# Performance work log

Measured on AMD Instinct MI355X. Metric: run time of the kernel, lower is better.

## Reference

```python
import math
import jax, jax.numpy as jnp
import numpy as np

B, L, D, H, DFF, T, V = 512, 128, 128, 4, 256, 2048, 20000
LN_EPS = 1e-5
LOG_SIGMA0 = math.log(0.1)


def _keygen(base):
    c = [0]
    def nk():
        k = jax.random.fold_in(base, c[0]); c[0] += 1
        return k
    return nk


def bayes_linear(x, wmu, wls, bmu, bls, nk):
    # weight = mu + exp(log_sigma) * eps (fresh eps every call, as in BayesLinear.forward)
    w = wmu + jnp.exp(wls) * jax.random.normal(nk(), wmu.shape, wmu.dtype)
    b = bmu + jnp.exp(bls) * jax.random.normal(nk(), bmu.shape, bmu.dtype)
    return jnp.einsum('...d,od->...o', x, w) + b


def layer_norm(x, g, b):
    m = x.mean(-1, keepdims=True)
    v = ((x - m) ** 2).mean(-1, keepdims=True)
    return (x - m) / jnp.sqrt(v + LN_EPS) * g + b


def mha(q, k, v, wmu, wls, bmu, bls, nk):
    # wmu: [4, D, D] for q, k, v, o projections
    dk = D // H
    def proj(x, i):
        return bayes_linear(x, wmu[i], wls[i], bmu[i], bls[i], nk)
    def split(x):
        return x.reshape(B, L, H, dk).transpose(0, 2, 1, 3)
    Q, K, Vh = split(proj(q, 0)), split(proj(k, 1)), split(proj(v, 2))
    probs = jax.nn.softmax(jnp.einsum('bhqd,bhkd->bhqk', Q, K) / math.sqrt(dk), axis=-1)
    out = jnp.einsum('bhqk,bhkd->bhqd', probs, Vh).transpose(0, 2, 1, 3).reshape(B, L, D)
    return bayes_linear(out, wmu[3], wls[3], bmu[3], bls[3], nk)


def setup_inputs() -> dict:
    key = jax.random.key(0)
    ks = iter(jax.random.split(key, 64))
    def u(shape, fan_in):
        s = 1.0 / math.sqrt(fan_in)
        return jax.random.uniform(next(ks), shape, jnp.float32, -s, s)
    def ls(shape):
        return jnp.full(shape, LOG_SIGMA0, jnp.float32)
    return dict(
        event_set=jax.random.randint(next(ks), (B, L), 0, V),
        time=jax.random.uniform(next(ks), (B, L), jnp.float32),
        mask=jax.random.randint(next(ks), (B, L), 0, L),
        set_size=jax.random.randint(next(ks), (B,), 1, L),
        emb=jax.random.normal(next(ks), (V, D), jnp.float32),
        dec_wmu=u((2, 8, D, D), D), dec_wls=ls((2, 8, D, D)),
        dec_bmu=u((2, 8, D), D), dec_bls=ls((2, 8, D)),
        ffn1_wmu=u((2, DFF, D), D), ffn1_wls=ls((2, DFF, D)),
        ffn1_bmu=u((2, DFF), D), ffn1_bls=ls((2, DFF)),
        ffn2_wmu=u((2, D, DFF), DFF), ffn2_wls=ls((2, D, DFF)),
        ffn2_bmu=u((2, D), DFF), ffn2_bls=ls((2, D)),
        ln_g=jnp.ones((2, 3, D), jnp.float32), ln_b=jnp.zeros((2, 3, D), jnp.float32),
        alpha_wmu=u((5, T, D), D), alpha_wls=ls((5, T, D)),
        alpha_bmu=u((5, T), D), alpha_bls=ls((5, T)),
        at_wmu=u((5, 1, D), D), at_wls=ls((5, 1, D)),
        at_bmu=u((5, 1), D), at_bls=ls((5, 1)),
        em_w=u((5, T, D), D), em_b=u((5, T), D),
        es_w=u((5, T, D), D), es_b=u((5, T), D),
        tm_w=u((5, 1, D), D), tm_b=u((5, 1), D),
        ts_w=u((5, 1, D), D), ts_b=u((5, 1), D),
    )


def reference(event_set, time, mask, set_size, emb,
              dec_wmu, dec_wls, dec_bmu, dec_bls,
              ffn1_wmu, ffn1_wls, ffn1_bmu, ffn1_bls,
              ffn2_wmu, ffn2_wls, ffn2_bmu, ffn2_bls,
              ln_g, ln_b, alpha_wmu, alpha_wls, alpha_bmu, alpha_bls,
              at_wmu, at_wls, at_bmu, at_bls,
              em_w, em_b, es_w, es_b, tm_w, tm_b, ts_w, ts_b):
    nk = _keygen(jax.random.key(42))
    x = emb[event_set]                                     # [B, L, D]
    # sinusoidal positional encoding driven by `mask` (integer positions)
    pos = mask.astype(jnp.float32)
    div = jnp.exp(jnp.arange(D, dtype=jnp.float32) * (-math.log(10000.0) / D))
    ang = pos[..., None] * div                             # [B, L, D]
    pos_enc = jnp.where((mask % 2 == 0)[..., None], jnp.sin(ang), jnp.cos(ang))
    inp_x = x + pos_enc
    # two decoder layers: self-attn on x, cross-attn against inp_x (dropout = eval identity)
    for l in range(2):
        a = mha(x, x, x, dec_wmu[l, :4], dec_wls[l, :4], dec_bmu[l, :4], dec_bls[l, :4], nk)
        x = layer_norm(x + a, ln_g[l, 0], ln_b[l, 0])
        a = mha(x, inp_x, inp_x, dec_wmu[l, 4:], dec_wls[l, 4:], dec_bmu[l, 4:], dec_bls[l, 4:], nk)
        x = layer_norm(x + a, ln_g[l, 1], ln_b[l, 1])
        h1 = jax.nn.relu(bayes_linear(x, ffn1_wmu[l], ffn1_wls[l], ffn1_bmu[l], ffn1_bls[l], nk))
        f = bayes_linear(h1, ffn2_wmu[l], ffn2_wls[l], ffn2_bmu[l], ffn2_bls[l], nk)
        x = layer_norm(x + f, ln_g[l, 2], ln_b[l, 2])
    h = x[:, 0, :]                                          # [B, D]
    # 5 Bayesian alpha heads -> softmax over mixture dim (vectorized over k)
    aw = alpha_wmu + jnp.exp(alpha_wls) * jax.random.normal(nk(), alpha_wmu.shape)
    ab = alpha_bmu + jnp.exp(alpha_bls) * jax.random.normal(nk(), alpha_bmu.shape)
    alpha = jax.nn.softmax(jnp.einsum('bd,ktd->btk', h, aw) + ab.T[None], axis=2)   # [B, T, 5]
    atw = at_wmu + jnp.exp(at_wls) * jax.random.normal(nk(), at_wmu.shape)
    atb = at_bmu + jnp.exp(at_bls) * jax.random.normal(nk(), at_bmu.shape)
    alpha_t = jax.nn.softmax(jnp.einsum('bd,kd->bk', h, atw[:, 0]) + atb[:, 0][None], axis=1)  # [B, 5]
    # mixture of 5 reparameterized Gaussian predictors (plain Linears)
    means = jnp.einsum('bd,ktd->bkt', h, em_w) + em_b[None]          # [B, 5, T]
    stds = jnp.exp(jnp.einsum('bd,ktd->bkt', h, es_w) + es_b[None])
    noise_e = jax.random.normal(nk(), (B, 5, T))
    event_pred = jnp.sum(jnp.swapaxes(alpha, 1, 2) * (means + stds * noise_e), axis=1)   # [B, T]
    tmeans = jnp.einsum('bd,kd->bk', h, tm_w[:, 0]) + tm_b[:, 0][None]                   # [B, 5]
    tstds = jnp.exp(jnp.einsum('bd,kd->bk', h, ts_w[:, 0]) + ts_b[:, 0][None])
    noise_t = jax.random.normal(nk(), (B, 5))
    time_pred = jnp.sum(alpha_t * (tmeans + tstds * noise_t), axis=1, keepdims=True)     # [B, 1]
    return event_pred, time_pred
```

## Files before the change

### kernel.cpp

```cpp
#include <hip/hip_runtime.h>
#include <cstdint>
#include <cstddef>


#define NB   512
#define NL   128
#define ND   128
#define NH   4
#define NDFF 256
#define NT   2048
#define BL   (NB * NL)

typedef __attribute__((ext_vector_type(8))) short bf16x8;
typedef __attribute__((ext_vector_type(4))) float f32x4;

#define MFMA16(a, b, c) __builtin_amdgcn_mfma_f32_16x16x32_bf16((a), (b), (c), 0, 0, 0)

__host__ __device__ __forceinline__ void tf2x32(uint32_t k0, uint32_t k1,
                                                uint32_t x0, uint32_t x1,
                                                uint32_t& o0, uint32_t& o1)
{
  const uint32_t ks2 = k0 ^ k1 ^ 0x1BD11BDAu;
  x0 += k0; x1 += k1;
#define TF_RND(r) { x0 += x1; x1 = (x1 << (r)) | (x1 >> (32 - (r))); x1 ^= x0; }
  TF_RND(13) TF_RND(15) TF_RND(26) TF_RND(6)
  x0 += k1;  x1 += ks2 + 1u;
  TF_RND(17) TF_RND(29) TF_RND(16) TF_RND(24)
  x0 += ks2; x1 += k0 + 2u;
  TF_RND(13) TF_RND(15) TF_RND(26) TF_RND(6)
  x0 += k0;  x1 += k1 + 3u;
  TF_RND(17) TF_RND(29) TF_RND(16) TF_RND(24)
  x0 += k1;  x1 += ks2 + 4u;
  TF_RND(13) TF_RND(15) TF_RND(26) TF_RND(6)
  x0 += ks2; x1 += k0 + 5u;
#undef TF_RND
  o0 = x0; o1 = x1;
}

__device__ __forceinline__ float erfinv32(float x)
{
  float w = -log1pf(-__fmul_rn(x, x));
  float p;
  if (w < 5.0f) {
    w = w - 2.5f;
    p = 2.81022636e-08f;
    p = __fadd_rn( 3.43273939e-07f, __fmul_rn(p, w));
    p = __fadd_rn(-3.5233877e-06f,  __fmul_rn(p, w));
    p = __fadd_rn(-4.39150654e-06f, __fmul_rn(p, w));
    p = __fadd_rn( 0.00021858087f,  __fmul_rn(p, w));
    p = __fadd_rn(-0.00125372503f,  __fmul_rn(p, w));
    p = __fadd_rn(-0.00417768164f,  __fmul_rn(p, w));
    p = __fadd_rn( 0.246640727f,    __fmul_rn(p, w));
    p = __fadd_rn( 1.50140941f,     __fmul_rn(p, w));
  } else {
    w = sqrtf(w) - 3.0f;
    p = -0.000200214257f;
    p = __fadd_rn( 0.000100950558f, __fmul_rn(p, w));
    p = __fadd_rn( 0.00134934322f,  __fmul_rn(p, w));
    p = __fadd_rn(-0.00367342844f,  __fmul_rn(p, w));
    p = __fadd_rn( 0.00573950773f,  __fmul_rn(p, w));
    p = __fadd_rn(-0.0076224613f,   __fmul_rn(p, w));
    p = __fadd_rn( 0.00943887047f,  __fmul_rn(p, w));
    p = __fadd_rn( 1.00167406f,     __fmul_rn(p, w));
    p = __fadd_rn( 2.83297682f,     __fmul_rn(p, w));
  }
  return __fmul_rn(p, x);
}

__device__ __forceinline__ float bits_to_normal(uint32_t bits)
{
  const float lo = -0.99999994f;
  float f = __uint_as_float((bits >> 9) | 0x3F800000u) - 1.0f;
  float u = __fadd_rn(__fmul_rn(f, 2.0f), lo);
  u = fmaxf(lo, u);
  return __fmul_rn(1.41421356f, erfinv32(u));
}

__device__ __forceinline__ float jax_normal_idx(uint32_t k0, uint32_t k1, uint32_t idx)
{
  uint32_t o0, o1;
  tf2x32(k0, k1, 0u, idx, o0, o1);
  return bits_to_normal(o0 ^ o1);
}

__device__ __forceinline__ ushort f2bf(float f)
{
  uint32_t u = __float_as_uint(f);
  u += 0x7fffu + ((u >> 16) & 1u);
  return (ushort)(u >> 16);
}

#define SA_DECB 262144
#define SA_F1W  264192
#define SA_F1B  329728
#define SA_F2W  330240
#define SA_F2B  395776
#define SA_AW   396032
#define SA_AB   1706752
#define SA_ATW  1716992
#define SA_ATB  1717632
#define SA_TOT  1717637

#define BW_DEC  0
#define BW_F1   262144
#define BW_F2   327680
#define BW_AW   393216
#define BW_TOT  1703936

#define BF_DECB 0
#define BF_F1B  2048
#define BF_F2B  2560
#define BF_AB   2816
#define BF_ATW  13056
#define BF_ATB  13696
#define BF_TOT  13701

__global__ __launch_bounds__(256) void sample_all_kernel(
    const float* __restrict__ dec_wmu, const float* __restrict__ dec_wls,
    const float* __restrict__ dec_bmu, const float* __restrict__ dec_bls,
    const float* __restrict__ f1_wmu,  const float* __restrict__ f1_wls,
    const float* __restrict__ f1_bmu,  const float* __restrict__ f1_bls,
    const float* __restrict__ f2_wmu,  const float* __restrict__ f2_wls,
    const float* __restrict__ f2_bmu,  const float* __restrict__ f2_bls,
    const float* __restrict__ a_wmu,   const float* __restrict__ a_wls,
    const float* __restrict__ a_bmu,   const float* __restrict__ a_bls,
    const float* __restrict__ at_wmu,  const float* __restrict__ at_wls,
    const float* __restrict__ at_bmu,  const float* __restrict__ at_bls,
    ushort* __restrict__ wbf, float* __restrict__ wf32)
{
  const int i = blockIdx.x * 256 + threadIdx.x;
  if (i >= SA_TOT) return;
  const float* mu; const float* ls;
  uint32_t c, idx;
  int bf_dst = -1, f32_dst = -1;
  if (i < SA_DECB) {
    int s = i >> 14;
    mu = dec_wmu + i; ls = dec_wls + i;
    c = 2u * s + (s >= 8 ? 4u : 0u); idx = (uint32_t)(i & 16383);
    bf_dst = BW_DEC + i;
  } else if (i < SA_F1W) {
    int t = i - SA_DECB; int s = t >> 7;
    mu = dec_bmu + t; ls = dec_bls + t;
    c = 2u * s + 1u + (s >= 8 ? 4u : 0u); idx = (uint32_t)(t & 127);
    f32_dst = BF_DECB + t;
  } else if (i < SA_F1B) {
    int t = i - SA_F1W; int s = t >> 15;
    mu = f1_wmu + t; ls = f1_wls + t;
    c = 16u + 20u * s; idx = (uint32_t)(t & 32767);
    bf_dst = BW_F1 + t;
  } else if (i < SA_F2W) {
    int t = i - SA_F1B; int s = t >> 8;
    mu = f1_bmu + t; ls = f1_bls + t;
    c = 17u + 20u * s; idx = (uint32_t)(t & 255);
    f32_dst = BF_F1B + t;
  } else if (i < SA_F2B) {
    int t = i - SA_F2W; int s = t >> 15;
    mu = f2_wmu + t; ls = f2_wls + t;
    c = 18u + 20u * s; idx = (uint32_t)(t & 32767);
    bf_dst = BW_F2 + t;
  } else if (i < SA_AW) {
    int t = i - SA_F2B; int s = t >> 7;
    mu = f2_bmu + t; ls = f2_bls + t;
    c = 19u + 20u * s; idx = (uint32_t)(t & 127);
    f32_dst = BF_F2B + t;
  } else if (i < SA_AB) {
    int t = i - SA_AW;
    mu = a_wmu + t; ls = a_wls + t; c = 40u; idx = (uint32_t)t;
    bf_dst = BW_AW + t;
  } else if (i < SA_ATW) {
    int t = i - SA_AB;
    mu = a_bmu + t; ls = a_bls + t; c = 41u; idx = (uint32_t)t;
    f32_dst = BF_AB + t;
  } else if (i < SA_ATB) {
    int t = i - SA_ATW;
    mu = at_wmu + t; ls = at_wls + t; c = 42u; idx = (uint32_t)t;
    f32_dst = BF_ATW + t;
  } else {
    int t = i - SA_ATB;
    mu = at_bmu + t; ls = at_bls + t; c = 43u; idx = (uint32_t)t;
    f32_dst = BF_ATB + t;
  }
  uint32_t k0, k1;
  tf2x32(0u, 42u, 0u, c, k0, k1);
  float v = mu[0] + expf(ls[0]) * jax_normal_idx(k0, k1, idx);
  if (bf_dst >= 0) wbf[bf_dst] = f2bf(v);
  else             wf32[f32_dst] = v;
}

#define STR 136

__global__ __launch_bounds__(512, 2) void decoder_mega_kernel(
    const int* __restrict__ ev, const int* __restrict__ mask,
    const float* __restrict__ emb,
    const ushort* __restrict__ WBF, const float* __restrict__ WF32,
    const float* __restrict__ lng_all, const float* __restrict__ lnb_all,
    float* __restrict__ Xh, ushort* __restrict__ Hb)
{
  __shared__ ushort WL[128][STR];
  __shared__ ushort Kt[128][STR];
  __shared__ ushort Vt[128][STR];
  __shared__ ushort Xb[128][STR];
  __shared__ ushort Ps[128][72];

  const int b = blockIdx.x;
  const int tid = threadIdx.x;
  const int w = tid >> 6, l = tid & 63;
  const int g = l >> 4, r16 = l & 15;
  const f32x4 zero = {0.f, 0.f, 0.f, 0.f};

  auto stageS = [&](ushort (*dst)[STR], const ushort* src, int srcStride) {
#pragma unroll
    for (int it = 0; it < 4; ++it) {
      int ci = tid + it * 512;
      int row = ci >> 4, q = ci & 15;
      *(bf16x8*)&dst[row][q * 8] = *(const bf16x8*)(src + (size_t)row * srcStride + q * 8);
    }
  };

  float xreg[8][4];
  {
    int ecr[4];
#pragma unroll
    for (int r = 0; r < 4; ++r) ecr[r] = ev[b * NL + 16 * w + 4 * g + r];
#pragma unroll
    for (int c = 0; c < 8; ++c)
#pragma unroll
      for (int r = 0; r < 4; ++r) {
        float x = emb[(size_t)ecr[r] * ND + 16 * c + r16];
        xreg[c][r] = x;
        Xb[16 * w + 4 * g + r][16 * c + r16] = f2bf(x);
      }
  }
  bf16x8 inpx[4];
  {
    const int row = 16 * w + r16;
    const int ea = ev[b * NL + row];
    const int mk = mask[b * NL + row];
    const bool even = (mk & 1) == 0;
    const float fm = (float)mk;
#pragma unroll
    for (int ks = 0; ks < 4; ++ks) {
      float4 x0 = *(const float4*)(emb + (size_t)ea * ND + 32 * ks + 8 * g);
      float4 x1 = *(const float4*)(emb + (size_t)ea * ND + 32 * ks + 8 * g + 4);
      float xs[8] = {x0.x, x0.y, x0.z, x0.w, x1.x, x1.y, x1.z, x1.w};
      bf16x8 v;
#pragma unroll
      for (int e = 0; e < 8; ++e) {
        int d = 32 * ks + 8 * g + e;
        float div = expf((float)d * (float)(-9.210340371976184 / 128.0));
        float ang = fm * div;
        float pe = even ? sinf(ang) : cosf(ang);
        v[e] = (short)f2bf(xs[e] + pe);
      }
      inpx[ks] = v;
    }
  }

#pragma unroll 1
  for (int st = 0; st < 6; ++st) {
    const int lay = st / 3, m = st - 3 * lay;
    const float* lng = lng_all + (size_t)(lay * 3 + m) * ND;
    const float* lnb = lnb_all + (size_t)(lay * 3 + m) * ND;
    f32x4 acc2[8];
#pragma unroll
    for (int c = 0; c < 8; ++c) acc2[c] = zero;
    float bo[8];

    __syncthreads();
    if (m < 2) {
      const int s0 = lay * 8 + m * 4;
      const ushort* W4 = WBF + BW_DEC + (size_t)s0 * 16384;
      const float*  B4 = WF32 + BF_DECB + (size_t)s0 * 128;

      stageS(WL, W4, 128);
      __syncthreads();
      f32x4 qacc[8];
#pragma unroll
      for (int c = 0; c < 8; ++c) qacc[c] = zero;
#pragma unroll
      for (int ks = 0; ks < 4; ++ks) {
        bf16x8 a = *(const bf16x8*)&Xb[16 * w + r16][32 * ks + 8 * g];
#pragma unroll
        for (int c = 0; c < 8; ++c) {
          bf16x8 wv = *(const bf16x8*)&WL[16 * c + r16][32 * ks + 8 * g];
          qacc[c] = MFMA16(a, wv, qacc[c]);
        }
      }
      __syncthreads();
      stageS(WL, W4 + 16384, 128);
      __syncthreads();
      {
        f32x4 kacc[8];
#pragma unroll
        for (int c = 0; c < 8; ++c) kacc[c] = zero;
#pragma unroll
        for (int ks = 0; ks < 4; ++ks) {
          bf16x8 a = (m == 0) ? *(const bf16x8*)&Xb[16 * w + r16][32 * ks + 8 * g]
                              : inpx[ks];
#pragma unroll
          for (int c = 0; c < 8; ++c) {
            bf16x8 wv = *(const bf16x8*)&WL[16 * c + r16][32 * ks + 8 * g];
            kacc[c] = MFMA16(a, wv, kacc[c]);
          }
        }
#pragma unroll
        for (int c = 0; c < 8; ++c) {
          float kb = B4[128 + 16 * c + r16];
#pragma unroll
          for (int r = 0; r < 4; ++r)
            Kt[16 * w + 4 * g + r][16 * c + r16] = f2bf(kacc[c][r] + kb);
        }
      }
      __syncthreads();
      stageS(WL, W4 + 2 * 16384, 128);
      __syncthreads();
      {
        f32x4 vacc[8];
#pragma unroll
        for (int c = 0; c < 8; ++c) vacc[c] = zero;
#pragma unroll
        for (int ks = 0; ks < 4; ++ks) {
          bf16x8 a = (m == 0) ? *(const bf16x8*)&Xb[16 * w + r16][32 * ks + 8 * g]
                              : inpx[ks];
#pragma unroll
          for (int c = 0; c < 8; ++c) {
            bf16x8 wv = *(const bf16x8*)&WL[16 * c + r16][32 * ks + 8 * g];
            vacc[c] = MFMA16(a, wv, vacc[c]);
          }
        }
#pragma unroll
        for (int c = 0; c < 8; ++c) {
          float vb = B4[256 + 16 * c + r16];
#pragma unroll
          for (int r = 0; r < 4; ++r)
            Vt[16 * c + r16][16 * w + 4 * g + r] = f2bf(vacc[c][r] + vb);
        }
      }
      __syncthreads();
#pragma unroll
      for (int c = 0; c < 8; ++c) {
        float qb = B4[16 * c + r16];
#pragma unroll
        for (int r = 0; r < 4; ++r)
          WL[16 * w + 4 * g + r][16 * c + r16] = f2bf(qacc[c][r] + qb);
      }
      __syncthreads();

      const float scale = 0.1767766952966369f;
      f32x4 oacc[4][2];
#pragma unroll
      for (int h = 0; h < 4; ++h) { oacc[h][0] = zero; oacc[h][1] = zero; }
#pragma unroll 1
      for (int h = 0; h < 4; ++h) {
        bf16x8 qa = *(const bf16x8*)&WL[16 * w + r16][32 * h + 8 * g];
        f32x4 s[8];
#pragma unroll
        for (int c = 0; c < 8; ++c) {
          bf16x8 kv = *(const bf16x8*)&Kt[16 * c + r16][32 * h + 8 * g];
          s[c] = MFMA16(qa, kv, zero);
        }
        float pv[4][8];
#pragma unroll
        for (int r = 0; r < 4; ++r) {
          float v[8]; float mx = -1e30f;
#pragma unroll
          for (int c = 0; c < 8; ++c) { v[c] = s[c][r] * scale; mx = fmaxf(mx, v[c]); }
#pragma unroll
          for (int o = 1; o < 16; o <<= 1) mx = fmaxf(mx, __shfl_xor(mx, o));
          float sum = 0.f;
#pragma unroll
          for (int c = 0; c < 8; ++c) { v[c] = __expf(v[c] - mx); sum += v[c]; }
#pragma unroll
          for (int o = 1; o < 16; o <<= 1) sum += __shfl_xor(sum, o);
          float inv = 1.0f / sum;
#pragma unroll
          for (int c = 0; c < 8; ++c) pv[r][c] = v[c] * inv;
        }
#pragma unroll
        for (int kc = 0; kc < 4; ++kc) {
          const int po = (kc & 1) * 32;
#pragma unroll
          for (int c2 = 0; c2 < 2; ++c2)
#pragma unroll
            for (int r = 0; r < 4; ++r)
              Ps[16 * w + 4 * g + r][po + 16 * c2 + r16] = f2bf(pv[r][2 * kc + c2]);
          bf16x8 pa = *(const bf16x8*)&Ps[16 * w + r16][po + 8 * g];
#pragma unroll
          for (int cc = 0; cc < 2; ++cc) {
            bf16x8 vv = *(const bf16x8*)&Vt[32 * h + 16 * cc + r16][32 * kc + 8 * g];
            oacc[h][cc] = MFMA16(pa, vv, oacc[h][cc]);
          }
        }
      }
      __syncthreads();
#pragma unroll
      for (int h = 0; h < 4; ++h)
#pragma unroll
        for (int cc = 0; cc < 2; ++cc)
#pragma unroll
          for (int r = 0; r < 4; ++r)
            Kt[16 * w + 4 * g + r][32 * h + 16 * cc + r16] = f2bf(oacc[h][cc][r]);
      stageS(WL, W4 + 3 * 16384, 128);
      __syncthreads();
#pragma unroll
      for (int ks = 0; ks < 4; ++ks) {
        bf16x8 a = *(const bf16x8*)&Kt[16 * w + r16][32 * ks + 8 * g];
#pragma unroll
        for (int c = 0; c < 8; ++c) {
          bf16x8 wv = *(const bf16x8*)&WL[16 * c + r16][32 * ks + 8 * g];
          acc2[c] = MFMA16(a, wv, acc2[c]);
        }
      }
#pragma unroll
      for (int c = 0; c < 8; ++c) bo[c] = B4[384 + 16 * c + r16];
    } else {
      const ushort* W1 = WBF + BW_F1 + (size_t)lay * 32768;
      const ushort* W2 = WBF + BW_F2 + (size_t)lay * 32768;
      const float*  B1 = WF32 + BF_F1B + (size_t)lay * 256;
      const float*  B2 = WF32 + BF_F2B + (size_t)lay * 128;
      stageS(WL, W1, 128);
      stageS(Kt, W1 + (size_t)128 * 128, 128);
      __syncthreads();
      f32x4 acc1[16];
#pragma unroll
      for (int c = 0; c < 16; ++c) acc1[c] = zero;
#pragma unroll
      for (int ks = 0; ks < 4; ++ks) {
        bf16x8 a = *(const bf16x8*)&Xb[16 * w + r16][32 * ks + 8 * g];
#pragma unroll
        for (int c = 0; c < 8; ++c) {
          bf16x8 w1v = *(const bf16x8*)&WL[16 * c + r16][32 * ks + 8 * g];
          acc1[c] = MFMA16(a, w1v, acc1[c]);
          bf16x8 w2v = *(const bf16x8*)&Kt[16 * c + r16][32 * ks + 8 * g];
          acc1[8 + c] = MFMA16(a, w2v, acc1[8 + c]);
        }
      }
      __syncthreads();
#pragma unroll
      for (int c = 0; c < 16; ++c) {
        float bb = B1[16 * c + r16];
#pragma unroll
        for (int r = 0; r < 4; ++r) {
          float o = fmaxf(acc1[c][r] + bb, 0.f);
          if (c < 8) WL[16 * w + 4 * g + r][16 * c + r16] = f2bf(o);
          else       Kt[16 * w + 4 * g + r][16 * (c - 8) + r16] = f2bf(o);
        }
      }
      stageS(Vt, W2, 256);
      __syncthreads();
#pragma unroll
      for (int ks = 0; ks < 4; ++ks) {
        bf16x8 a = *(const bf16x8*)&WL[16 * w + r16][32 * ks + 8 * g];
#pragma unroll
        for (int c = 0; c < 8; ++c) {
          bf16x8 wv = *(const bf16x8*)&Vt[16 * c + r16][32 * ks + 8 * g];
          acc2[c] = MFMA16(a, wv, acc2[c]);
        }
      }
      __syncthreads();
      stageS(Vt, W2 + 128, 256);
      __syncthreads();
#pragma unroll
      for (int ks = 0; ks < 4; ++ks) {
        bf16x8 a = *(const bf16x8*)&Kt[16 * w + r16][32 * ks + 8 * g];
#pragma unroll
        for (int c = 0; c < 8; ++c) {
          bf16x8 wv = *(const bf16x8*)&Vt[16 * c + r16][32 * ks + 8 * g];
          acc2[c] = MFMA16(a, wv, acc2[c]);
        }
      }
#pragma unroll
      for (int c = 0; c < 8; ++c) bo[c] = B2[16 * c + r16];
    }

    float gg[8], lb[8];
#pragma unroll
    for (int c = 0; c < 8; ++c) { gg[c] = lng[16 * c + r16]; lb[c] = lnb[16 * c + r16]; }
#pragma unroll
    for (int r = 0; r < 4; ++r) {
      float xv[8];
#pragma unroll
      for (int c = 0; c < 8; ++c) xv[c] = acc2[c][r] + bo[c] + xreg[c][r];
      float s = 0.f;
#pragma unroll
      for (int c = 0; c < 8; ++c) s += xv[c];
#pragma unroll
      for (int o = 1; o < 16; o <<= 1) s += __shfl_xor(s, o);
      float mean = s * (1.0f / 128.0f);
      float q = 0.f;
#pragma unroll
      for (int c = 0; c < 8; ++c) { float d = xv[c] - mean; q += d * d; }
#pragma unroll
      for (int o = 1; o < 16; o <<= 1) q += __shfl_xor(q, o);
      float inv = 1.0f / sqrtf(q * (1.0f / 128.0f) + 1e-5f);
#pragma unroll
      for (int c = 0; c < 8; ++c) {
        float o = (xv[c] - mean) * inv * gg[c] + lb[c];
        xreg[c][r] = o;
        Xb[16 * w + 4 * g + r][16 * c + r16] = f2bf(o);
      }
    }
  }

  if (w == 0 && g == 0) {
#pragma unroll
    for (int c = 0; c < 8; ++c) {
      Xh[(size_t)b * ND + 16 * c + r16] = xreg[c][0];
      Hb[(size_t)b * ND + 16 * c + r16] = f2bf(xreg[c][0]);
    }
  }
}

template<int WFP32>
__global__ __launch_bounds__(256) void head_gemm(
    const ushort* __restrict__ A,
    const ushort* __restrict__ Wb16, const float* __restrict__ Wf32,
    const float* __restrict__ bias, float* __restrict__ C, int ldc)
{
  __shared__ char smem[128 * 132 * 4];
  ushort (*Wl)[STR] = (ushort(*)[STR])smem;
  float  (*Cl)[132] = (float(*)[132])smem;

  const int tid = threadIdx.x;
  const int bn = blockIdx.x * 128;
  const int bm = blockIdx.y * 128;
  const int w = tid >> 6, l = tid & 63;
  const int r16 = l & 15, g = l >> 4;
  const f32x4 zero = {0.f, 0.f, 0.f, 0.f};

#pragma unroll
  for (int it = 0; it < 8; ++it) {
    int ci = tid + it * 256;
    int row = ci >> 4, q = ci & 15;
    if (WFP32) {
      float4 v0 = *(const float4*)(Wf32 + (size_t)(bn + row) * 128 + q * 8);
      float4 v1 = *(const float4*)(Wf32 + (size_t)(bn + row) * 128 + q * 8 + 4);
      bf16x8 o;
      o[0] = f2bf(v0.x); o[1] = f2bf(v0.y); o[2] = f2bf(v0.z); o[3] = f2bf(v0.w);
      o[4] = f2bf(v1.x); o[5] = f2bf(v1.y); o[6] = f2bf(v1.z); o[7] = f2bf(v1.w);
      *(bf16x8*)&Wl[row][q * 8] = o;
    } else {
      *(bf16x8*)&Wl[row][q * 8] =
          *(const bf16x8*)(Wb16 + (size_t)(bn + row) * 128 + q * 8);
    }
  }
  __syncthreads();

  f32x4 acc[2][8];
#pragma unroll
  for (int t = 0; t < 2; ++t)
#pragma unroll
    for (int c = 0; c < 8; ++c) acc[t][c] = zero;
#pragma unroll
  for (int ks = 0; ks < 4; ++ks) {
    bf16x8 a[2];
#pragma unroll
    for (int t = 0; t < 2; ++t)
      a[t] = *(const bf16x8*)(A + (size_t)(bm + 32 * w + 16 * t + r16) * 128
                              + 32 * ks + 8 * g);
    bf16x8 wv[8];
#pragma unroll
    for (int c = 0; c < 8; ++c)
      wv[c] = *(const bf16x8*)&Wl[16 * c + r16][32 * ks + 8 * g];
#pragma unroll
    for (int t = 0; t < 2; ++t)
#pragma unroll
      for (int c = 0; c < 8; ++c)
        acc[t][c] = MFMA16(a[t], wv[c], acc[t][c]);
  }

  float bcol[8];
#pragma unroll
  for (int c = 0; c < 8; ++c) bcol[c] = bias[bn + 16 * c + r16];
  __syncthreads();

#pragma unroll
  for (int t = 0; t < 2; ++t)
#pragma unroll
    for (int c = 0; c < 8; ++c)
#pragma unroll
      for (int r = 0; r < 4; ++r)
        Cl[32 * w + 16 * t + 4 * g + r][16 * c + r16] = acc[t][c][r] + bcol[c];
  __syncthreads();
#pragma unroll
  for (int i = 0; i < 16; ++i) {
    int ci = l + 64 * i;
    int row = 32 * w + (ci >> 5), q = ci & 31;
    float4 v = *(const float4*)&Cl[row][4 * q];
    *(float4*)(C + (size_t)(bm + row) * ldc + bn + 4 * q) = v;
  }
}

__global__ __launch_bounds__(256) void event_head_kernel(
    const float* __restrict__ LA, const float* __restrict__ MB,
    const float* __restrict__ SB, float* __restrict__ out,
    uint32_t k0, uint32_t k1)
{
  int i = blockIdx.x * 256 + threadIdx.x;
  if (i >= NB * NT) return;
  int b = i >> 11, t = i & (NT - 1);
  size_t base = (size_t)b * (5 * NT) + t;
  float lg[5];
  float mx = -1e30f;
#pragma unroll
  for (int k = 0; k < 5; ++k) { lg[k] = LA[base + (size_t)k * NT]; mx = fmaxf(mx, lg[k]); }
  float se = 0.f;
#pragma unroll
  for (int k = 0; k < 5; ++k) { lg[k] = expf(lg[k] - mx); se += lg[k]; }
  float inv = 1.0f / se;
  float acc = 0.f;
#pragma unroll
  for (int k = 0; k < 5; ++k) {
    float nz = jax_normal_idx(k0, k1, (uint32_t)((b * 5 + k) * NT + t));
    float mean = MB[base + (size_t)k * NT];
    float sd   = expf(SB[base + (size_t)k * NT]);
    acc += (lg[k] * inv) * (mean + sd * nz);
  }
  out[i] = acc;
}

__global__ __launch_bounds__(64) void time_head_kernel(
    const float* __restrict__ Xh, const float* __restrict__ atw,
    const float* __restrict__ atb, const float* __restrict__ tmw,
    const float* __restrict__ tmb, const float* __restrict__ tsw,
    const float* __restrict__ tsb, float* __restrict__ out,
    uint32_t k0, uint32_t k1)
{
  const int b = blockIdx.x;
  const int l = threadIdx.x;
  const float* h = Xh + (size_t)b * ND;
  const float h0 = h[l], h1 = h[l + 64];
  float lg[5], tm[5], tsl[5];
#pragma unroll
  for (int k = 0; k < 5; ++k) {
    float s0 = fmaf(h0, atw[k * ND + l], h1 * atw[k * ND + l + 64]);
    float s1 = fmaf(h0, tmw[k * ND + l], h1 * tmw[k * ND + l + 64]);
    float s2 = fmaf(h0, tsw[k * ND + l], h1 * tsw[k * ND + l + 64]);
#pragma unroll
    for (int o = 32; o; o >>= 1) {
      s0 += __shfl_xor(s0, o);
      s1 += __shfl_xor(s1, o);
      s2 += __shfl_xor(s2, o);
    }
    lg[k] = s0 + atb[k]; tm[k] = s1 + tmb[k]; tsl[k] = s2 + tsb[k];
  }
  if (l == 0) {
    float mx = lg[0];
    for (int k = 1; k < 5; ++k) mx = fmaxf(mx, lg[k]);
    float se = 0.f;
    for (int k = 0; k < 5; ++k) { lg[k] = expf(lg[k] - mx); se += lg[k]; }
    float acc = 0.f;
    for (int k = 0; k < 5; ++k) {
      float nz = jax_normal_idx(k0, k1, (uint32_t)(b * 5 + k));
      acc += (lg[k] / se) * (tm[k] + expf(tsl[k]) * nz);
    }
    out[b] = acc;
  }
}

extern "C" void kernel_launch(void* const* d_in, const int* in_sizes, int n_in,
                              void* d_out, int out_size, void* d_ws, size_t ws_size,
                              hipStream_t stream)
{
  (void)in_sizes; (void)n_in; (void)out_size; (void)ws_size;

  const int*   ev      = (const int*)d_in[0];
  const int*   mask    = (const int*)d_in[2];
  const float* emb     = (const float*)d_in[4];
  const float* dec_wmu = (const float*)d_in[5];
  const float* dec_wls = (const float*)d_in[6];
  const float* dec_bmu = (const float*)d_in[7];
  const float* dec_bls = (const float*)d_in[8];
  const float* f1_wmu  = (const float*)d_in[9];
  const float* f1_wls  = (const float*)d_in[10];
  const float* f1_bmu  = (const float*)d_in[11];
  const float* f1_bls  = (const float*)d_in[12];
  const float* f2_wmu  = (const float*)d_in[13];
  const float* f2_wls  = (const float*)d_in[14];
  const float* f2_bmu  = (const float*)d_in[15];
  const float* f2_bls  = (const float*)d_in[16];
  const float* ln_g    = (const float*)d_in[17];
  const float* ln_b    = (const float*)d_in[18];
  const float* a_wmu   = (const float*)d_in[19];
  const float* a_wls   = (const float*)d_in[20];
  const float* a_bmu   = (const float*)d_in[21];
  const float* a_bls   = (const float*)d_in[22];
  const float* at_wmu  = (const float*)d_in[23];
  const float* at_wls  = (const float*)d_in[24];
  const float* at_bmu  = (const float*)d_in[25];
  const float* at_bls  = (const float*)d_in[26];
  const float* em_w    = (const float*)d_in[27];
  const float* em_b    = (const float*)d_in[28];
  const float* es_w    = (const float*)d_in[29];
  const float* es_b    = (const float*)d_in[30];
  const float* tm_w    = (const float*)d_in[31];
  const float* tm_b    = (const float*)d_in[32];
  const float* ts_w    = (const float*)d_in[33];
  const float* ts_b    = (const float*)d_in[34];

  float* ws = (float*)d_ws;
  const size_t HN = (size_t)NB * 5 * NT;
  float*  LA   = ws;
  float*  MBo  = LA + HN;
  float*  SBo  = MBo + HN;
  ushort* WBF  = (ushort*)(SBo + HN);
  float*  WF32 = SBo + HN + BW_TOT / 2;
  ushort* Hb   = (ushort*)(WF32 + BF_TOT + 3);
  float*  Xh   = (float*)(Hb + (size_t)NB * ND);

  uint32_t fk0[46], fk1[46];
  for (uint32_t c = 0; c < 46; ++c) tf2x32(0u, 42u, 0u, c, fk0[c], fk1[c]);

  sample_all_kernel<<<dim3((SA_TOT + 255) / 256), dim3(256), 0, stream>>>(
      dec_wmu, dec_wls, dec_bmu, dec_bls,
      f1_wmu, f1_wls, f1_bmu, f1_bls,
      f2_wmu, f2_wls, f2_bmu, f2_bls,
      a_wmu, a_wls, a_bmu, a_bls,
      at_wmu, at_wls, at_bmu, at_bls, WBF, WF32);

  decoder_mega_kernel<<<dim3(NB), dim3(512), 0, stream>>>(
      ev, mask, emb, WBF, WF32, ln_g, ln_b, Xh, Hb);

  head_gemm<0><<<dim3(80, 4), dim3(256), 0, stream>>>(
      Hb, WBF + BW_AW, nullptr, WF32 + BF_AB, LA, 5 * NT);
  head_gemm<1><<<dim3(80, 4), dim3(256), 0, stream>>>(
      Hb, nullptr, em_w, em_b, MBo, 5 * NT);
  head_gemm<1><<<dim3(80, 4), dim3(256), 0, stream>>>(
      Hb, nullptr, es_w, es_b, SBo, 5 * NT);

  float* out = (float*)d_out;
  event_head_kernel<<<dim3((NB * NT) / 256), dim3(256), 0, stream>>>(
      LA, MBo, SBo, out, fk0[44], fk1[44]);
  time_head_kernel<<<dim3(NB), dim3(64), 0, stream>>>(
      Xh, WF32 + BF_ATW, WF32 + BF_ATB, tm_w, tm_b, ts_w, ts_b,
      out + (size_t)NB * NT, fk0[45], fk1[45]);
}
```

Measured before the change: 309.6 us.

## Fuse head GEMMs with mixture epilogue and read decoder weights directly from global

```diff
diff --git a/kernel.cpp b/kernel.cpp
--- a/kernel.cpp
+++ b/kernel.cpp
@@ -189,14 +189,13 @@
 
 #define STR 136
 
-__global__ __launch_bounds__(512, 2) void decoder_mega_kernel(
+__global__ __launch_bounds__(512, 1) void decoder_mega_kernel(
     const int* __restrict__ ev, const int* __restrict__ mask,
     const float* __restrict__ emb,
     const ushort* __restrict__ WBF, const float* __restrict__ WF32,
     const float* __restrict__ lng_all, const float* __restrict__ lnb_all,
     float* __restrict__ Xh, ushort* __restrict__ Hb)
 {
-  __shared__ ushort WL[128][STR];
   __shared__ ushort Kt[128][STR];
   __shared__ ushort Vt[128][STR];
   __shared__ ushort Xb[128][STR];
@@ -207,15 +206,6 @@
   const int w = tid >> 6, l = tid & 63;
   const int g = l >> 4, r16 = l & 15;
   const f32x4 zero = {0.f, 0.f, 0.f, 0.f};
-
-  auto stageS = [&](ushort (*dst)[STR], const ushort* src, int srcStride) {
-#pragma unroll
-    for (int it = 0; it < 4; ++it) {
-      int ci = tid + it * 512;
-      int row = ci >> 4, q = ci & 15;
-      *(bf16x8*)&dst[row][q * 8] = *(const bf16x8*)(src + (size_t)row * srcStride + q * 8);
-    }
-  };
 
   float xreg[8][4];
   {
@@ -266,29 +256,13 @@
     for (int c = 0; c < 8; ++c) acc2[c] = zero;
     float bo[8];
 
-    __syncthreads();
     if (m < 2) {
       const int s0 = lay * 8 + m * 4;
       const ushort* W4 = WBF + BW_DEC + (size_t)s0 * 16384;
       const float*  B4 = WF32 + BF_DECB + (size_t)s0 * 128;
 
-      stageS(WL, W4, 128);
       __syncthreads();
-      f32x4 qacc[8];
-#pragma unroll
-      for (int c = 0; c < 8; ++c) qacc[c] = zero;
-#pragma unroll
-      for (int ks = 0; ks < 4; ++ks) {
-        bf16x8 a = *(const bf16x8*)&Xb[16 * w + r16][32 * ks + 8 * g];
-#pragma unroll
-        for (int c = 0; c < 8; ++c) {
-          bf16x8 wv = *(const bf16x8*)&WL[16 * c + r16][32 * ks + 8 * g];
-          qacc[c] = MFMA16(a, wv, qacc[c]);
-        }
-      }
-      __syncthreads();
-      stageS(WL, W4 + 16384, 128);
-      __syncthreads();
+
       {
         f32x4 kacc[8];
 #pragma unroll
@@ -299,7 +273,8 @@
                               : inpx[ks];
 #pragma unroll
           for (int c = 0; c < 8; ++c) {
-            bf16x8 wv = *(const bf16x8*)&WL[16 * c + r16][32 * ks + 8 * g];
+            bf16x8 wv = *(const bf16x8*)(W4 + 16384 + (size_t)(16 * c + r16) * 128
+                                         + 32 * ks + 8 * g);
             kacc[c] = MFMA16(a, wv, kacc[c]);
           }
         }
@@ -311,9 +286,6 @@
             Kt[16 * w + 4 * g + r][16 * c + r16] = f2bf(kacc[c][r] + kb);
         }
       }
-      __syncthreads();
-      stageS(WL, W4 + 2 * 16384, 128);
-      __syncthreads();
       {
         f32x4 vacc[8];
 #pragma unroll
@@ -324,25 +296,41 @@
                               : inpx[ks];
 #pragma unroll
           for (int c = 0; c < 8; ++c) {
-            bf16x8 wv = *(const bf16x8*)&WL[16 * c + r16][32 * ks + 8 * g];
+            bf16x8 wv = *(const bf16x8*)(W4 + 2 * 16384 + (size_t)(16 * c + r16) * 128
+                                         + 32 * ks + 8 * g);
             vacc[c] = MFMA16(a, wv, vacc[c]);
           }
         }
 #pragma unroll
         for (int c = 0; c < 8; ++c) {
           float vb = B4[256 + 16 * c + r16];
+          ushort4 pk;
+          pk.x = f2bf(vacc[c][0] + vb); pk.y = f2bf(vacc[c][1] + vb);
+          pk.z = f2bf(vacc[c][2] + vb); pk.w = f2bf(vacc[c][3] + vb);
+          *(ushort4*)&Vt[16 * c + r16][16 * w + 4 * g] = pk;
+        }
+      }
+      {
+        f32x4 qacc[8];
+#pragma unroll
+        for (int c = 0; c < 8; ++c) qacc[c] = zero;
+#pragma unroll
+        for (int ks = 0; ks < 4; ++ks) {
+          bf16x8 a = *(const bf16x8*)&Xb[16 * w + r16][32 * ks + 8 * g];
+#pragma unroll
+          for (int c = 0; c < 8; ++c) {
+            bf16x8 wv = *(const bf16x8*)(W4 + (size_t)(16 * c + r16) * 128
+                                         + 32 * ks + 8 * g);
+            qacc[c] = MFMA16(a, wv, qacc[c]);
+          }
+        }
+#pragma unroll
+        for (int c = 0; c < 8; ++c) {
+          float qb = B4[16 * c + r16];
 #pragma unroll
           for (int r = 0; r < 4; ++r)
-            Vt[16 * c + r16][16 * w + 4 * g + r] = f2bf(vacc[c][r] + vb);
-        }
-      }
-      __syncthreads();
-#pragma unroll
-      for (int c = 0; c < 8; ++c) {
-        float qb = B4[16 * c + r16];
-#pragma unroll
-        for (int r = 0; r < 4; ++r)
-          WL[16 * w + 4 * g + r][16 * c + r16] = f2bf(qacc[c][r] + qb);
+            Xb[16 * w + 4 * g + r][16 * c + r16] = f2bf(qacc[c][r] + qb);
+        }
       }
       __syncthreads();
 
@@ -352,7 +340,7 @@
       for (int h = 0; h < 4; ++h) { oacc[h][0] = zero; oacc[h][1] = zero; }
 #pragma unroll 1
       for (int h = 0; h < 4; ++h) {
-        bf16x8 qa = *(const bf16x8*)&WL[16 * w + r16][32 * h + 8 * g];
+        bf16x8 qa = *(const bf16x8*)&Xb[16 * w + r16][32 * h + 8 * g];
         f32x4 s[8];
 #pragma unroll
         for (int c = 0; c < 8; ++c) {
@@ -393,6 +381,7 @@
         }
       }
       __syncthreads();
+
 #pragma unroll
       for (int h = 0; h < 4; ++h)
 #pragma unroll
@@ -400,14 +389,13 @@
 #pragma unroll
           for (int r = 0; r < 4; ++r)
             Kt[16 * w + 4 * g + r][32 * h + 16 * cc + r16] = f2bf(oacc[h][cc][r]);
-      stageS(WL, W4 + 3 * 16384, 128);
-      __syncthreads();
 #pragma unroll
       for (int ks = 0; ks < 4; ++ks) {
         bf16x8 a = *(const bf16x8*)&Kt[16 * w + r16][32 * ks + 8 * g];
 #pragma unroll
         for (int c = 0; c < 8; ++c) {
-          bf16x8 wv = *(const bf16x8*)&WL[16 * c + r16][32 * ks + 8 * g];
+          bf16x8 wv = *(const bf16x8*)(W4 + 3 * 16384 + (size_t)(16 * c + r16) * 128
+                                       + 32 * ks + 8 * g);
           acc2[c] = MFMA16(a, wv, acc2[c]);
         }
       }
@@ -418,9 +406,7 @@
       const ushort* W2 = WBF + BW_F2 + (size_t)lay * 32768;
       const float*  B1 = WF32 + BF_F1B + (size_t)lay * 256;
       const float*  B2 = WF32 + BF_F2B + (size_t)lay * 128;
-      stageS(WL, W1, 128);
-      stageS(Kt, W1 + (size_t)128 * 128, 128);
-      __syncthreads();
+
       f32x4 acc1[16];
 #pragma unroll
       for (int c = 0; c < 16; ++c) acc1[c] = zero;
@@ -428,44 +414,31 @@
       for (int ks = 0; ks < 4; ++ks) {
         bf16x8 a = *(const bf16x8*)&Xb[16 * w + r16][32 * ks + 8 * g];
 #pragma unroll
-        for (int c = 0; c < 8; ++c) {
-          bf16x8 w1v = *(const bf16x8*)&WL[16 * c + r16][32 * ks + 8 * g];
-          acc1[c] = MFMA16(a, w1v, acc1[c]);
-          bf16x8 w2v = *(const bf16x8*)&Kt[16 * c + r16][32 * ks + 8 * g];
-          acc1[8 + c] = MFMA16(a, w2v, acc1[8 + c]);
-        }
-      }
-      __syncthreads();
+        for (int c = 0; c < 16; ++c) {
+          bf16x8 wv = *(const bf16x8*)(W1 + (size_t)(16 * c + r16) * 128
+                                       + 32 * ks + 8 * g);
+          acc1[c] = MFMA16(a, wv, acc1[c]);
+        }
+      }
 #pragma unroll
       for (int c = 0; c < 16; ++c) {
         float bb = B1[16 * c + r16];
 #pragma unroll
         for (int r = 0; r < 4; ++r) {
           float o = fmaxf(acc1[c][r] + bb, 0.f);
-          if (c < 8) WL[16 * w + 4 * g + r][16 * c + r16] = f2bf(o);
-          else       Kt[16 * w + 4 * g + r][16 * (c - 8) + r16] = f2bf(o);
-        }
-      }
-      stageS(Vt, W2, 256);
-      __syncthreads();
-#pragma unroll
-      for (int ks = 0; ks < 4; ++ks) {
-        bf16x8 a = *(const bf16x8*)&WL[16 * w + r16][32 * ks + 8 * g];
+          if (c < 8) Kt[16 * w + 4 * g + r][16 * c + r16] = f2bf(o);
+          else       Vt[16 * w + 4 * g + r][16 * (c - 8) + r16] = f2bf(o);
+        }
+      }
+#pragma unroll
+      for (int ks = 0; ks < 8; ++ks) {
+        bf16x8 a = (ks < 4)
+          ? *(const bf16x8*)&Kt[16 * w + r16][32 * ks + 8 * g]
+          : *(const bf16x8*)&Vt[16 * w + r16][32 * (ks - 4) + 8 * g];
 #pragma unroll
         for (int c = 0; c < 8; ++c) {
-          bf16x8 wv = *(const bf16x8*)&Vt[16 * c + r16][32 * ks + 8 * g];
-          acc2[c] = MFMA16(a, wv, acc2[c]);
-        }
-      }
-      __syncthreads();
-      stageS(Vt, W2 + 128, 256);
-      __syncthreads();
-#pragma unroll
-      for (int ks = 0; ks < 4; ++ks) {
-        bf16x8 a = *(const bf16x8*)&Kt[16 * w + r16][32 * ks + 8 * g];
-#pragma unroll
-        for (int c = 0; c < 8; ++c) {
-          bf16x8 wv = *(const bf16x8*)&Vt[16 * c + r16][32 * ks + 8 * g];
+          bf16x8 wv = *(const bf16x8*)(W2 + (size_t)(16 * c + r16) * 256
+                                       + 32 * ks + 8 * g);
           acc2[c] = MFMA16(a, wv, acc2[c]);
         }
       }
@@ -511,112 +484,85 @@
   }
 }
 
-template<int WFP32>
-__global__ __launch_bounds__(256) void head_gemm(
-    const ushort* __restrict__ A,
-    const ushort* __restrict__ Wb16, const float* __restrict__ Wf32,
-    const float* __restrict__ bias, float* __restrict__ C, int ldc)
-{
-  __shared__ char smem[128 * 132 * 4];
-  ushort (*Wl)[STR] = (ushort(*)[STR])smem;
-  float  (*Cl)[132] = (float(*)[132])smem;
-
+__global__ __launch_bounds__(256) void head_fused_kernel(
+    const ushort* __restrict__ Hb,
+    const ushort* __restrict__ AW, const float* __restrict__ ABs,
+    const float* __restrict__ em_w, const float* __restrict__ em_b,
+    const float* __restrict__ es_w, const float* __restrict__ es_b,
+    float* __restrict__ out, uint32_t k0, uint32_t k1)
+{
+  const int t0 = blockIdx.x * 16;
+  const int bm = blockIdx.y * 128;
   const int tid = threadIdx.x;
-  const int bn = blockIdx.x * 128;
-  const int bm = blockIdx.y * 128;
   const int w = tid >> 6, l = tid & 63;
-  const int r16 = l & 15, g = l >> 4;
+  const int g = l >> 4, r16 = l & 15;
   const f32x4 zero = {0.f, 0.f, 0.f, 0.f};
-
-#pragma unroll
-  for (int it = 0; it < 8; ++it) {
-    int ci = tid + it * 256;
-    int row = ci >> 4, q = ci & 15;
-    if (WFP32) {
-      float4 v0 = *(const float4*)(Wf32 + (size_t)(bn + row) * 128 + q * 8);
-      float4 v1 = *(const float4*)(Wf32 + (size_t)(bn + row) * 128 + q * 8 + 4);
-      bf16x8 o;
-      o[0] = f2bf(v0.x); o[1] = f2bf(v0.y); o[2] = f2bf(v0.z); o[3] = f2bf(v0.w);
-      o[4] = f2bf(v1.x); o[5] = f2bf(v1.y); o[6] = f2bf(v1.z); o[7] = f2bf(v1.w);
-      *(bf16x8*)&Wl[row][q * 8] = o;
-    } else {
-      *(bf16x8*)&Wl[row][q * 8] =
-          *(const bf16x8*)(Wb16 + (size_t)(bn + row) * 128 + q * 8);
-    }
-  }
-  __syncthreads();
-
-  f32x4 acc[2][8];
+  const int tl = t0 + r16;
+
+  f32x4 aA[2][5], aE[2][5], aS[2][5];
 #pragma unroll
   for (int t = 0; t < 2; ++t)
 #pragma unroll
-    for (int c = 0; c < 8; ++c) acc[t][c] = zero;
+    for (int k = 0; k < 5; ++k) { aA[t][k] = zero; aE[t][k] = zero; aS[t][k] = zero; }
+
 #pragma unroll
   for (int ks = 0; ks < 4; ++ks) {
-    bf16x8 a[2];
-#pragma unroll
-    for (int t = 0; t < 2; ++t)
-      a[t] = *(const bf16x8*)(A + (size_t)(bm + 32 * w + 16 * t + r16) * 128
-                              + 32 * ks + 8 * g);
-    bf16x8 wv[8];
-#pragma unroll
-    for (int c = 0; c < 8; ++c)
-      wv[c] = *(const bf16x8*)&Wl[16 * c + r16][32 * ks + 8 * g];
-#pragma unroll
-    for (int t = 0; t < 2; ++t)
-#pragma unroll
-      for (int c = 0; c < 8; ++c)
-        acc[t][c] = MFMA16(a[t], wv[c], acc[t][c]);
-  }
-
-  float bcol[8];
-#pragma unroll
-  for (int c = 0; c < 8; ++c) bcol[c] = bias[bn + 16 * c + r16];
-  __syncthreads();
+    bf16x8 a0 = *(const bf16x8*)(Hb + (size_t)(bm + 32 * w + r16) * 128 + 32 * ks + 8 * g);
+    bf16x8 a1 = *(const bf16x8*)(Hb + (size_t)(bm + 32 * w + 16 + r16) * 128 + 32 * ks + 8 * g);
+#pragma unroll
+    for (int k = 0; k < 5; ++k) {
+      const size_t R = (size_t)(k * NT + tl) * 128 + 32 * ks + 8 * g;
+      bf16x8 wa = *(const bf16x8*)(AW + R);
+      aA[0][k] = MFMA16(a0, wa, aA[0][k]);
+      aA[1][k] = MFMA16(a1, wa, aA[1][k]);
+      float4 e0 = *(const float4*)(em_w + R);
+      float4 e1 = *(const float4*)(em_w + R + 4);
+      bf16x8 we;
+      we[0] = f2bf(e0.x); we[1] = f2bf(e0.y); we[2] = f2bf(e0.z); we[3] = f2bf(e0.w);
+      we[4] = f2bf(e1.x); we[5] = f2bf(e1.y); we[6] = f2bf(e1.z); we[7] = f2bf(e1.w);
+      aE[0][k] = MFMA16(a0, we, aE[0][k]);
+      aE[1][k] = MFMA16(a1, we, aE[1][k]);
+      float4 s0 = *(const float4*)(es_w + R);
+      float4 s1 = *(const float4*)(es_w + R + 4);
+      bf16x8 wsv;
+      wsv[0] = f2bf(s0.x); wsv[1] = f2bf(s0.y); wsv[2] = f2bf(s0.z); wsv[3] = f2bf(s0.w);
+      wsv[4] = f2bf(s1.x); wsv[5] = f2bf(s1.y); wsv[6] = f2bf(s1.z); wsv[7] = f2bf(s1.w);
+      aS[0][k] = MFMA16(a0, wsv, aS[0][k]);
+      aS[1][k] = MFMA16(a1, wsv, aS[1][k]);
+    }
+  }
+
+  float bA[5], bE[5], bS[5];
+#pragma unroll
+  for (int k = 0; k < 5; ++k) {
+    bA[k] = ABs[k * NT + tl];
+    bE[k] = em_b[k * NT + tl];
+    bS[k] = es_b[k * NT + tl];
+  }
 
 #pragma unroll
   for (int t = 0; t < 2; ++t)
 #pragma unroll
-    for (int c = 0; c < 8; ++c)
-#pragma unroll
-      for (int r = 0; r < 4; ++r)
-        Cl[32 * w + 16 * t + 4 * g + r][16 * c + r16] = acc[t][c][r] + bcol[c];
-  __syncthreads();
-#pragma unroll
-  for (int i = 0; i < 16; ++i) {
-    int ci = l + 64 * i;
-    int row = 32 * w + (ci >> 5), q = ci & 31;
-    float4 v = *(const float4*)&Cl[row][4 * q];
-    *(float4*)(C + (size_t)(bm + row) * ldc + bn + 4 * q) = v;
-  }
-}
-
-__global__ __launch_bounds__(256) void event_head_kernel(
-    const float* __restrict__ LA, const float* __restrict__ MB,
-    const float* __restrict__ SB, float* __restrict__ out,
-    uint32_t k0, uint32_t k1)
-{
-  int i = blockIdx.x * 256 + threadIdx.x;
-  if (i >= NB * NT) return;
-  int b = i >> 11, t = i & (NT - 1);
-  size_t base = (size_t)b * (5 * NT) + t;
-  float lg[5];
-  float mx = -1e30f;
-#pragma unroll
-  for (int k = 0; k < 5; ++k) { lg[k] = LA[base + (size_t)k * NT]; mx = fmaxf(mx, lg[k]); }
-  float se = 0.f;
-#pragma unroll
-  for (int k = 0; k < 5; ++k) { lg[k] = expf(lg[k] - mx); se += lg[k]; }
-  float inv = 1.0f / se;
-  float acc = 0.f;
-#pragma unroll
-  for (int k = 0; k < 5; ++k) {
-    float nz = jax_normal_idx(k0, k1, (uint32_t)((b * 5 + k) * NT + t));
-    float mean = MB[base + (size_t)k * NT];
-    float sd   = expf(SB[base + (size_t)k * NT]);
-    acc += (lg[k] * inv) * (mean + sd * nz);
-  }
-  out[i] = acc;
+    for (int r = 0; r < 4; ++r) {
+      const int brow = bm + 32 * w + 16 * t + 4 * g + r;
+      float lg[5];
+      float mx = -1e30f;
+#pragma unroll
+      for (int k = 0; k < 5; ++k) { lg[k] = aA[t][k][r] + bA[k]; mx = fmaxf(mx, lg[k]); }
+      float se = 0.f;
+#pragma unroll
+      for (int k = 0; k < 5; ++k) { lg[k] = expf(lg[k] - mx); se += lg[k]; }
+      const float inv = 1.0f / se;
+      float acc = 0.f;
+#pragma unroll
+      for (int k = 0; k < 5; ++k) {
+        float nz = jax_normal_idx(k0, k1, (uint32_t)((brow * 5 + k) * NT + tl));
+        float mean = aE[t][k][r] + bE[k];
+        float sd   = expf(aS[t][k][r] + bS[k]);
+        acc += (lg[k] * inv) * (mean + sd * nz);
+      }
+      out[(size_t)brow * NT + tl] = acc;
+    }
 }
 
 __global__ __launch_bounds__(64) void time_head_kernel(
@@ -699,12 +645,8 @@
   const float* ts_b    = (const float*)d_in[34];
 
   float* ws = (float*)d_ws;
-  const size_t HN = (size_t)NB * 5 * NT;
-  float*  LA   = ws;
-  float*  MBo  = LA + HN;
-  float*  SBo  = MBo + HN;
-  ushort* WBF  = (ushort*)(SBo + HN);
-  float*  WF32 = SBo + HN + BW_TOT / 2;
+  ushort* WBF  = (ushort*)ws;
+  float*  WF32 = ws + BW_TOT / 2;
   ushort* Hb   = (ushort*)(WF32 + BF_TOT + 3);
   float*  Xh   = (float*)(Hb + (size_t)NB * ND);
 
@@ -721,16 +663,10 @@
   decoder_mega_kernel<<<dim3(NB), dim3(512), 0, stream>>>(
       ev, mask, emb, WBF, WF32, ln_g, ln_b, Xh, Hb);
 
-  head_gemm<0><<<dim3(80, 4), dim3(256), 0, stream>>>(
-      Hb, WBF + BW_AW, nullptr, WF32 + BF_AB, LA, 5 * NT);
-  head_gemm<1><<<dim3(80, 4), dim3(256), 0, stream>>>(
-      Hb, nullptr, em_w, em_b, MBo, 5 * NT);
-  head_gemm<1><<<dim3(80, 4), dim3(256), 0, stream>>>(
-      Hb, nullptr, es_w, es_b, SBo, 5 * NT);
-
   float* out = (float*)d_out;
-  event_head_kernel<<<dim3((NB * NT) / 256), dim3(256), 0, stream>>>(
-      LA, MBo, SBo, out, fk0[44], fk1[44]);
+  head_fused_kernel<<<dim3(NT / 16, 4), dim3(256), 0, stream>>>(
+      Hb, WBF + BW_AW, WF32 + BF_AB, em_w, em_b, es_w, es_b,
+      out, fk0[44], fk1[44]);
   time_head_kernel<<<dim3(NB), dim3(64), 0, stream>>>(
       Xh, WF32 + BF_ATW, WF32 + BF_ATB, tm_w, tm_b, ts_w, ts_b,
       out + (size_t)NB * NT, fk0[45], fk1[45]);
```

Result: slower. 595.6 us (+92.4%).
